# Performance work log

Measured on AMD Instinct MI355X. Metric: run time of the kernel, lower is better.

The kernel has to match this reference:

```python
import jax, jax.numpy as jnp
import numpy as np

D_MODEL = 1024
N_HEADS = 16
HEAD_DIM = D_MODEL // N_HEADS
BATCH = 4
SEQ = 2048


def setup_inputs() -> dict:
    key = jax.random.key(0)
    ks = jax.random.split(key, 5)
    # Xavier uniform bound for square d_model x d_model weights
    bound = np.sqrt(6.0 / (D_MODEL + D_MODEL))
    x = jax.random.normal(ks[0], (BATCH, SEQ, D_MODEL), dtype=jnp.float32)
    attention_mask = jnp.ones((BATCH, SEQ), dtype=jnp.int32)
    wq = jax.random.uniform(ks[1], (D_MODEL, D_MODEL), jnp.float32, -bound, bound)
    wk = jax.random.uniform(ks[2], (D_MODEL, D_MODEL), jnp.float32, -bound, bound)
    wv = jax.random.uniform(ks[3], (D_MODEL, D_MODEL), jnp.float32, -bound, bound)
    wo = jax.random.uniform(ks[4], (D_MODEL, D_MODEL), jnp.float32, -bound, bound)
    return {"x": x, "attention_mask": attention_mask,
            "wq": wq, "wk": wk, "wv": wv, "wo": wo}


def reference(x, attention_mask, wq, wk, wv, wo):
    # x: (B, S, D). Linear weights stored torch-style (out, in): y = x @ W^T
    B, S, D = x.shape
    H, Hd = N_HEADS, HEAD_DIM
    scale = np.sqrt(Hd).astype(np.float32)

    def split_heads(t):  # (B,S,D) -> (B,H,S,Hd)
        return t.reshape(B, S, H, Hd).transpose(0, 2, 1, 3)

    q = split_heads(jnp.einsum('bsd,ed->bse', x, wq))
    k = split_heads(jnp.einsum('bsd,ed->bse', x, wk))
    v = split_heads(jnp.einsum('bsd,ed->bse', x, wv))

    scores = jnp.einsum('bhqd,bhkd->bhqk', q, k) / scale  # (B,H,S,S)

    causal = jnp.tril(jnp.ones((S, S), dtype=bool))  # True = keep
    keep = causal[None, None, :, :] & (attention_mask[:, None, None, :] != 0)
    scores = jnp.where(keep, scores, -jnp.inf)

    attn = jax.nn.softmax(scores, axis=-1)  # dropout: eval mode (identity)
    out = jnp.einsum('bhqk,bhkd->bhqd', attn, v)  # (B,H,S,Hd)
    out = out.transpose(0, 2, 1, 3).reshape(B, S, D)
    return jnp.einsum('bsd,ed->bse', out, wo)
```

## Files before the change

### kernel.cpp

```cpp
#include <hip/hip_runtime.h>
#include <cstdint>
#include <cstddef>

#define D_MODEL 1024
#define N_HEADS 16
#define HEAD_DIM 64
#define BATCH 4
#define SEQ 2048
#define M_TOTAL (BATCH * SEQ)

typedef __attribute__((ext_vector_type(8))) short bf16x8;
typedef __attribute__((ext_vector_type(4))) float f32x4;
typedef __attribute__((ext_vector_type(16))) float f32x16;

#define Q_SCALE 0.18033688011112042f

__device__ __forceinline__ unsigned short f2bu(float f) {
    union { float f; unsigned u; } x; x.f = f;
    unsigned r = x.u + 0x7FFFu + ((x.u >> 16) & 1u);
    return (unsigned short)(r >> 16);
}

__device__ __forceinline__ void async16(void* lds, const void* g) {
    __builtin_amdgcn_global_load_lds(
        (const __attribute__((address_space(1))) void*)g,
        (__attribute__((address_space(3))) void*)lds, 16, 0, 0);
}

__global__ __launch_bounds__(256) void cast_all(const float* __restrict__ x,
                                                const float* __restrict__ wq,
                                                const float* __restrict__ wk,
                                                const float* __restrict__ wv,
                                                const float* __restrict__ wo,
                                                unsigned short* __restrict__ dst) {
    const size_t NE = (size_t)M_TOTAL * D_MODEL;
    const size_t WE = (size_t)D_MODEL * D_MODEL;
    size_t i4 = (size_t)blockIdx.x * 256 + threadIdx.x;
    size_t e = i4 * 4;
    const float* src; size_t off;
    if (e < NE) { src = x; off = e; }
    else {
        size_t t = e - NE;
        int r = (int)(t / WE); off = t - (size_t)r * WE;
        src = (r == 0) ? wq : (r == 1) ? wk : (r == 2) ? wv : wo;
    }
    float4 v = *(const float4*)(src + off);
    ushort4 o;
    o.x = f2bu(v.x); o.y = f2bu(v.y); o.z = f2bu(v.z); o.w = f2bu(v.w);
    ((ushort4*)dst)[i4] = o;
}

__global__ __launch_bounds__(256) void qkv_gemm(const unsigned short* __restrict__ X,
                                                const unsigned short* __restrict__ W0,
                                                const unsigned short* __restrict__ W1,
                                                const unsigned short* __restrict__ W2,
                                                unsigned short* __restrict__ Y0,
                                                unsigned short* __restrict__ Y1,
                                                unsigned short* __restrict__ Vt) {
    __shared__ short As[128 * 32];
    __shared__ short Bs[128 * 32];

    const int sel = blockIdx.x >> 3;
    const unsigned short* W = (sel == 0) ? W0 : (sel == 1) ? W1 : W2;
    const float scl = (sel == 0) ? Q_SCALE : 1.0f;

    const int tid = threadIdx.x;
    const int w = tid >> 6, lane = tid & 63, quad = lane >> 4, l15 = lane & 15;
    const int wm = w & 1, wn = w >> 1;
    const int rowBase = blockIdx.y * 128;
    const int colBase = (blockIdx.x & 7) * 128;

    f32x4 acc[4][4];
#pragma unroll
    for (int mi = 0; mi < 4; ++mi)
#pragma unroll
        for (int ni = 0; ni < 4; ++ni)
#pragma unroll
            for (int e = 0; e < 4; ++e) acc[mi][ni][e] = 0.f;

    for (int k0 = 0; k0 < 1024; k0 += 32) {
        __syncthreads();
#pragma unroll
        for (int l = 0; l < 2; ++l) {
            int c = tid + l * 256;
            int row = c >> 2, ccs = c & 3;
            int cc = ccs ^ ((row >> 1) & 3);
            async16((char*)As + c * 16, X + (size_t)(rowBase + row) * 1024 + k0 + cc * 8);
            async16((char*)Bs + c * 16, W + (size_t)(colBase + row) * 1024 + k0 + cc * 8);
        }
        __syncthreads();

        bf16x8 a[4], b[4];
#pragma unroll
        for (int mi = 0; mi < 4; ++mi) {
            int r = wm * 64 + mi * 16 + l15;
            int slot = quad ^ ((r >> 1) & 3);
            a[mi] = *(const bf16x8*)&As[r * 32 + slot * 8];
        }
#pragma unroll
        for (int ni = 0; ni < 4; ++ni) {
            int r = wn * 64 + ni * 16 + l15;
            int slot = quad ^ ((r >> 1) & 3);
            b[ni] = *(const bf16x8*)&Bs[r * 32 + slot * 8];
        }
#pragma unroll
        for (int mi = 0; mi < 4; ++mi)
#pragma unroll
            for (int ni = 0; ni < 4; ++ni)
                acc[mi][ni] = __builtin_amdgcn_mfma_f32_16x16x32_bf16(a[mi], b[ni], acc[mi][ni], 0, 0, 0);
    }

    if (sel != 2) {
        unsigned short* Y = (sel == 0) ? Y0 : Y1;
#pragma unroll
        for (int mi = 0; mi < 4; ++mi)
#pragma unroll
            for (int ni = 0; ni < 4; ++ni)
#pragma unroll
                for (int reg = 0; reg < 4; ++reg) {
                    int row = rowBase + wm * 64 + mi * 16 + quad * 4 + reg;
                    int col = colBase + wn * 64 + ni * 16 + l15;
                    Y[(size_t)row * 1024 + col] = f2bu(acc[mi][ni][reg] * scl);
                }
    } else {
#pragma unroll
        for (int mi = 0; mi < 4; ++mi) {
            int row0 = rowBase + wm * 64 + mi * 16 + quad * 4;
            int bb = row0 >> 11;
            int s0 = row0 & 2047;
#pragma unroll
            for (int ni = 0; ni < 4; ++ni) {
                int col = colBase + wn * 64 + ni * 16 + l15;
                int hh = col >> 6, dd = col & 63;
                ushort4 pk;
                pk.x = f2bu(acc[mi][ni][0]); pk.y = f2bu(acc[mi][ni][1]);
                pk.z = f2bu(acc[mi][ni][2]); pk.w = f2bu(acc[mi][ni][3]);
                *(ushort4*)(Vt + (((size_t)bb * 16 + hh) * 64 + dd) * SEQ + s0) = pk;
            }
        }
    }
}

__global__ __launch_bounds__(256) void out_gemm(const unsigned short* __restrict__ X,
                                                const unsigned short* __restrict__ W,
                                                float* __restrict__ Y) {
    __shared__ short As[128 * 32];
    __shared__ short Bs[128 * 32];

    const int tid = threadIdx.x;
    const int w = tid >> 6, lane = tid & 63, quad = lane >> 4, l15 = lane & 15;
    const int wm = w & 1, wn = w >> 1;
    const int rowBase = blockIdx.y * 128;
    const int colBase = blockIdx.x * 128;

    f32x4 acc[4][4];
#pragma unroll
    for (int mi = 0; mi < 4; ++mi)
#pragma unroll
        for (int ni = 0; ni < 4; ++ni)
#pragma unroll
            for (int e = 0; e < 4; ++e) acc[mi][ni][e] = 0.f;

    for (int k0 = 0; k0 < 1024; k0 += 32) {
        __syncthreads();
#pragma unroll
        for (int l = 0; l < 2; ++l) {
            int c = tid + l * 256;
            int row = c >> 2, ccs = c & 3;
            int cc = ccs ^ ((row >> 1) & 3);
            async16((char*)As + c * 16, X + (size_t)(rowBase + row) * 1024 + k0 + cc * 8);
            async16((char*)Bs + c * 16, W + (size_t)(colBase + row) * 1024 + k0 + cc * 8);
        }
        __syncthreads();

        bf16x8 a[4], b[4];
#pragma unroll
        for (int mi = 0; mi < 4; ++mi) {
            int r = wm * 64 + mi * 16 + l15;
            int slot = quad ^ ((r >> 1) & 3);
            a[mi] = *(const bf16x8*)&As[r * 32 + slot * 8];
        }
#pragma unroll
        for (int ni = 0; ni < 4; ++ni) {
            int r = wn * 64 + ni * 16 + l15;
            int slot = quad ^ ((r >> 1) & 3);
            b[ni] = *(const bf16x8*)&Bs[r * 32 + slot * 8];
        }
#pragma unroll
        for (int mi = 0; mi < 4; ++mi)
#pragma unroll
            for (int ni = 0; ni < 4; ++ni)
                acc[mi][ni] = __builtin_amdgcn_mfma_f32_16x16x32_bf16(a[mi], b[ni], acc[mi][ni], 0, 0, 0);
    }

#pragma unroll
    for (int mi = 0; mi < 4; ++mi)
#pragma unroll
        for (int ni = 0; ni < 4; ++ni)
#pragma unroll
            for (int reg = 0; reg < 4; ++reg) {
                int row = rowBase + wm * 64 + mi * 16 + quad * 4 + reg;
                int col = colBase + wn * 64 + ni * 16 + l15;
                Y[(size_t)row * 1024 + col] = acc[mi][ni][reg];
            }
}

__global__ __launch_bounds__(256) void flash32(const unsigned short* __restrict__ Q,
                                               const unsigned short* __restrict__ K,
                                               const unsigned short* __restrict__ Vt,
                                               const int* __restrict__ mask,
                                               unsigned short* __restrict__ CTX) {
    __shared__ short lds[9216];
    __shared__ float biasS[64];
    __shared__ int allokS;
    __shared__ int okW[4];

    short* Ks = lds;
    short* Vs = lds + 4096;

    const int pid = blockIdx.x;
    const int bh = blockIdx.y;
    const int b = bh >> 4;
    const int tid = threadIdx.x;
    const int w = tid >> 6, lane = tid & 63, l31 = lane & 31, lane5 = lane >> 5;

    const size_t qkBase = (size_t)b * SEQ * D_MODEL + (size_t)(bh & 15) * HEAD_DIM;
    const size_t vtBase = (size_t)bh * HEAD_DIM * SEQ;

    {
        int ok = 1;
        for (int i = tid; i < SEQ; i += 256) ok &= (mask[b * SEQ + i] != 0);
        unsigned long long bal = __ballot(ok != 0);
        if (lane == 0) okW[w] = (bal == ~0ull) ? 1 : 0;
    }
    __syncthreads();
    const int allSeq = okW[0] & okW[1] & okW[2] & okW[3];

    int stp[2], stcc[2], stj[2];
#pragma unroll
    for (int l = 0; l < 2; ++l) {
        int c = tid + l * 256;
        int p = c >> 3, sl = c & 7;
        stp[l] = p;
        stcc[l] = sl ^ (p & 7);
        stj[l] = (p & 0x33) | ((p & 4) << 1) | ((p & 8) >> 1);
    }

    for (int phase = 0; phase < 2; ++phase) {
        const int qt = phase ? pid : 15 - pid;
        const int q0 = qt * 128;
        const int iq = q0 + w * 32 + l31;

        bf16x8 qf[4];
#pragma unroll
        for (int ks = 0; ks < 4; ++ks)
            qf[ks] = *(const bf16x8*)(Q + qkBase + (size_t)iq * D_MODEL + ks * 16 + lane5 * 8);

        float mv = -INFINITY, lv = 0.f;
        f32x16 Ot[2];
#pragma unroll
        for (int dt = 0; dt < 2; ++dt)
#pragma unroll
            for (int e = 0; e < 16; ++e) Ot[dt][e] = 0.f;

        const int ktmax = 2 * qt + 1;

        uint4 kreg[2], vreg[2];
        int mreg = 1;
        {
            const int k0 = 0;
#pragma unroll
            for (int l = 0; l < 2; ++l) {
                kreg[l] = *(const uint4*)(K + qkBase + (size_t)(k0 + stj[l]) * D_MODEL + stcc[l] * 8);
                vreg[l] = *(const uint4*)(Vt + vtBase + (size_t)stp[l] * SEQ + k0 + stcc[l] * 8);
            }
            if (!allSeq && tid < 64) mreg = mask[b * SEQ + k0 + tid];
        }

        for (int kt = 0; kt <= ktmax; ++kt) {
            const int k0 = kt * 64;
            __syncthreads();
#pragma unroll
            for (int l = 0; l < 2; ++l) {
                int c = tid + l * 256;
                *(uint4*)((char*)Ks + c * 16) = kreg[l];
                *(uint4*)((char*)Vs + c * 16) = vreg[l];
            }
            if (!allSeq && tid < 64) {
                biasS[tid] = mreg ? 0.f : -INFINITY;
                unsigned long long bal = __ballot(mreg != 0);
                if (tid == 0) allokS = (bal == ~0ull) ? 1 : 0;
            }
            if (kt < ktmax) {
                const int kn = k0 + 64;
#pragma unroll
                for (int l = 0; l < 2; ++l) {
                    kreg[l] = *(const uint4*)(K + qkBase + (size_t)(kn + stj[l]) * D_MODEL + stcc[l] * 8);
                    vreg[l] = *(const uint4*)(Vt + vtBase + (size_t)stp[l] * SEQ + kn + stcc[l] * 8);
                }
                if (!allSeq && tid < 64) mreg = mask[b * SEQ + kn + tid];
            }
            __syncthreads();

            if (64 * kt > q0 + 32 * w + 31) continue;

            f32x16 St[2];
#pragma unroll
            for (int T = 0; T < 2; ++T)
#pragma unroll
                for (int e = 0; e < 16; ++e) St[T][e] = 0.f;
            __builtin_amdgcn_s_setprio(1);
#pragma unroll
            for (int T = 0; T < 2; ++T)
#pragma unroll
                for (int ks = 0; ks < 4; ++ks) {
                    int p = T * 32 + l31;
                    int slot = (ks * 2 + lane5) ^ (p & 7);
                    bf16x8 a = *(const bf16x8*)&Ks[p * 64 + slot * 8];
                    St[T] = __builtin_amdgcn_mfma_f32_32x32x16_bf16(a, qf[ks], St[T], 0, 0, 0);
                }
            __builtin_amdgcn_s_setprio(0);

            const bool partial = (k0 + 63 > q0 + 32 * w);
            if (partial) {
#pragma unroll
                for (int T = 0; T < 2; ++T)
#pragma unroll
                    for (int r = 0; r < 16; ++r) {
                        int j = k0 + 32 * T + 16 * (r >> 3) + 8 * lane5 + (r & 7);
                        if (j > iq) St[T][r] = -INFINITY;
                    }
            }
            if (!allSeq && !allokS) {
#pragma unroll
                for (int T = 0; T < 2; ++T)
#pragma unroll
                    for (int r = 0; r < 16; ++r)
                        St[T][r] += biasS[32 * T + 16 * (r >> 3) + 8 * lane5 + (r & 7)];
            }

            float rm = -INFINITY;
#pragma unroll
            for (int T = 0; T < 2; ++T)
#pragma unroll
                for (int r = 0; r < 16; ++r) rm = fmaxf(rm, St[T][r]);
            rm = fmaxf(rm, __shfl_xor(rm, 32));
            float mn = fmaxf(mv, rm);
            if (mn > mv + 8.f) {
                float al = exp2f(mv - mn);
                lv *= al;
#pragma unroll
                for (int dt = 0; dt < 2; ++dt)
#pragma unroll
                    for (int e = 0; e < 16; ++e) Ot[dt][e] *= al;
                mv = mn;
            }
            float rs = 0.f;
#pragma unroll
            for (int T = 0; T < 2; ++T)
#pragma unroll
                for (int r = 0; r < 16; ++r) {
                    float pv = exp2f(St[T][r] - mv);
                    St[T][r] = pv;
                    rs += pv;
                }
            rs += __shfl_xor(rs, 32);
            lv += rs;

            bf16x8 pf[4];
#pragma unroll
            for (int t = 0; t < 4; ++t) {
                const int T = t >> 1, hb = t & 1;
                unsigned u0, u1, u2, u3;
                asm("v_cvt_pk_bf16_f32 %0, %1, %2" : "=v"(u0)
                    : "v"(St[T][hb * 8 + 0]), "v"(St[T][hb * 8 + 1]));
                asm("v_cvt_pk_bf16_f32 %0, %1, %2" : "=v"(u1)
                    : "v"(St[T][hb * 8 + 2]), "v"(St[T][hb * 8 + 3]));
                asm("v_cvt_pk_bf16_f32 %0, %1, %2" : "=v"(u2)
                    : "v"(St[T][hb * 8 + 4]), "v"(St[T][hb * 8 + 5]));
                asm("v_cvt_pk_bf16_f32 %0, %1, %2" : "=v"(u3)
                    : "v"(St[T][hb * 8 + 6]), "v"(St[T][hb * 8 + 7]));
                union { unsigned u[4]; bf16x8 v; } pk;
                pk.u[0] = u0; pk.u[1] = u1; pk.u[2] = u2; pk.u[3] = u3;
                pf[t] = pk.v;
            }

            __builtin_amdgcn_s_setprio(1);
#pragma unroll
            for (int dt = 0; dt < 2; ++dt)
#pragma unroll
                for (int t = 0; t < 4; ++t) {
                    int p = dt * 32 + l31;
                    int slot = (t * 2 + lane5) ^ (p & 7);
                    bf16x8 a = *(const bf16x8*)&Vs[p * 64 + slot * 8];
                    Ot[dt] = __builtin_amdgcn_mfma_f32_32x32x16_bf16(a, pf[t], Ot[dt], 0, 0, 0);
                }
            __builtin_amdgcn_s_setprio(0);
        }

        __syncthreads();
        const float inv = 1.f / lv;
#pragma unroll
        for (int dt = 0; dt < 2; ++dt)
#pragma unroll
            for (int k = 0; k < 8; ++k) {
                int r0 = 2 * k;
                int d = (r0 & 3) + 4 * lane5 + 8 * (r0 >> 2) + 32 * dt;
                unsigned lo = f2bu(Ot[dt][r0] * inv);
                unsigned hi = f2bu(Ot[dt][r0 + 1] * inv);
                *(unsigned*)&lds[(w * 32 + l31) * 72 + d] = lo | (hi << 16);
            }
        __syncthreads();
#pragma unroll
        for (int k = 0; k < 4; ++k) {
            int id = tid + k * 256;
            int r = id >> 3, cc = id & 7;
            uint4 v = *(const uint4*)&lds[r * 72 + cc * 8];
            *(uint4*)(CTX + qkBase + (size_t)(q0 + r) * D_MODEL + cc * 8) = v;
        }
    }
}

extern "C" void kernel_launch(void* const* d_in, const int* in_sizes, int n_in,
                              void* d_out, int out_size, void* d_ws, size_t ws_size,
                              hipStream_t stream) {
    const float* x  = (const float*)d_in[0];
    const int* mask = (const int*)d_in[1];
    const float* wq = (const float*)d_in[2];
    const float* wk = (const float*)d_in[3];
    const float* wv = (const float*)d_in[4];
    const float* wo = (const float*)d_in[5];
    float* out = (float*)d_out;

    const size_t NE = (size_t)M_TOTAL * D_MODEL;
    const size_t WE = (size_t)D_MODEL * D_MODEL;
    unsigned short* ws  = (unsigned short*)d_ws;
    unsigned short* xb  = ws;
    unsigned short* wqb = xb + NE;
    unsigned short* wkb = wqb + WE;
    unsigned short* wvb = wkb + WE;
    unsigned short* wob = wvb + WE;
    unsigned short* Qb  = wob + WE;
    unsigned short* Kb  = Qb + NE;
    unsigned short* Vtb = Kb + NE;
    unsigned short* CTX = Vtb + NE;

    cast_all<<<(int)((NE + 4 * WE) / 4 / 256), 256, 0, stream>>>(x, wq, wk, wv, wo, ws);

    qkv_gemm<<<dim3(24, M_TOTAL / 128), 256, 0, stream>>>(xb, wqb, wkb, wvb, Qb, Kb, Vtb);

    flash32<<<dim3(8, BATCH * N_HEADS), 256, 0, stream>>>(Qb, Kb, Vtb, mask, CTX);

    out_gemm<<<dim3(D_MODEL / 128, M_TOTAL / 128), 256, 0, stream>>>(CTX, wob, out);
}
```

Baseline: 309.3 us.

## Double-buffer K/V tiles in flash kernel and launch one block per query tile

```diff
diff --git a/kernel.cpp b/kernel.cpp
--- a/kernel.cpp
+++ b/kernel.cpp
@@ -210,16 +210,13 @@
                                                const unsigned short* __restrict__ Vt,
                                                const int* __restrict__ mask,
                                                unsigned short* __restrict__ CTX) {
-    __shared__ short lds[9216];
-    __shared__ float biasS[64];
-    __shared__ int allokS;
+    __shared__ short lds[16384];
+    __shared__ float biasS[2][64];
+    __shared__ int allokS[2];
     __shared__ int okW[4];
 
-    short* Ks = lds;
-    short* Vs = lds + 4096;
-
-    const int pid = blockIdx.x;
-    const int bh = blockIdx.y;
+    const int bh = blockIdx.x;
+    const int qt = 15 - (int)blockIdx.y;
     const int b = bh >> 4;
     const int tid = threadIdx.x;
     const int w = tid >> 6, lane = tid & 63, l31 = lane & 31, lane5 = lane >> 5;
@@ -246,178 +243,177 @@
         stj[l] = (p & 0x33) | ((p & 4) << 1) | ((p & 8) >> 1);
     }
 
-    for (int phase = 0; phase < 2; ++phase) {
-        const int qt = phase ? pid : 15 - pid;
-        const int q0 = qt * 128;
-        const int iq = q0 + w * 32 + l31;
-
-        bf16x8 qf[4];
-#pragma unroll
-        for (int ks = 0; ks < 4; ++ks)
-            qf[ks] = *(const bf16x8*)(Q + qkBase + (size_t)iq * D_MODEL + ks * 16 + lane5 * 8);
-
-        float mv = -INFINITY, lv = 0.f;
-        f32x16 Ot[2];
+    const int q0 = qt * 128;
+    const int iq = q0 + w * 32 + l31;
+
+    bf16x8 qf[4];
+#pragma unroll
+    for (int ks = 0; ks < 4; ++ks)
+        qf[ks] = *(const bf16x8*)(Q + qkBase + (size_t)iq * D_MODEL + ks * 16 + lane5 * 8);
+
+    float mv = -INFINITY, lv = 0.f;
+    f32x16 Ot[2];
+#pragma unroll
+    for (int dt = 0; dt < 2; ++dt)
+#pragma unroll
+        for (int e = 0; e < 16; ++e) Ot[dt][e] = 0.f;
+
+    const int ktmax = 2 * qt + 1;
+
+    uint4 kreg[2], vreg[2];
+    int mreg = 1;
+#pragma unroll
+    for (int l = 0; l < 2; ++l) {
+        kreg[l] = *(const uint4*)(K + qkBase + (size_t)stj[l] * D_MODEL + stcc[l] * 8);
+        vreg[l] = *(const uint4*)(Vt + vtBase + (size_t)stp[l] * SEQ + stcc[l] * 8);
+    }
+    if (!allSeq && tid < 64) mreg = mask[b * SEQ + tid];
+
+    for (int kt = 0; kt <= ktmax; ++kt) {
+        const int k0 = kt * 64;
+        const int buf = kt & 1;
+#pragma unroll
+        for (int l = 0; l < 2; ++l) {
+            int c = tid + l * 256;
+            *(uint4*)((char*)lds + buf * 8192 + c * 16) = kreg[l];
+            *(uint4*)((char*)lds + 16384 + buf * 8192 + c * 16) = vreg[l];
+        }
+        if (!allSeq && tid < 64) {
+            biasS[buf][tid] = mreg ? 0.f : -INFINITY;
+            unsigned long long bal = __ballot(mreg != 0);
+            if (tid == 0) allokS[buf] = (bal == ~0ull) ? 1 : 0;
+        }
+        if (kt < ktmax) {
+            const int kn = k0 + 64;
+#pragma unroll
+            for (int l = 0; l < 2; ++l) {
+                kreg[l] = *(const uint4*)(K + qkBase + (size_t)(kn + stj[l]) * D_MODEL + stcc[l] * 8);
+                vreg[l] = *(const uint4*)(Vt + vtBase + (size_t)stp[l] * SEQ + kn + stcc[l] * 8);
+            }
+            if (!allSeq && tid < 64) mreg = mask[b * SEQ + kn + tid];
+        }
+        __syncthreads();
+
+        if (64 * kt > q0 + 32 * w + 31) continue;
+
+        const short* Ks = lds + buf * 4096;
+        const short* Vs = lds + 8192 + buf * 4096;
+
+        f32x16 St[2];
+#pragma unroll
+        for (int T = 0; T < 2; ++T)
+#pragma unroll
+            for (int e = 0; e < 16; ++e) St[T][e] = 0.f;
+        __builtin_amdgcn_s_setprio(1);
+#pragma unroll
+        for (int T = 0; T < 2; ++T)
+#pragma unroll
+            for (int ks = 0; ks < 4; ++ks) {
+                int p = T * 32 + l31;
+                int slot = (ks * 2 + lane5) ^ (p & 7);
+                bf16x8 a = *(const bf16x8*)&Ks[p * 64 + slot * 8];
+                St[T] = __builtin_amdgcn_mfma_f32_32x32x16_bf16(a, qf[ks], St[T], 0, 0, 0);
+            }
+        __builtin_amdgcn_s_setprio(0);
+
+        const bool partial = (k0 + 63 > q0 + 32 * w);
+        if (partial) {
+#pragma unroll
+            for (int T = 0; T < 2; ++T)
+#pragma unroll
+                for (int r = 0; r < 16; ++r) {
+                    int j = k0 + 32 * T + 16 * (r >> 3) + 8 * lane5 + (r & 7);
+                    if (j > iq) St[T][r] = -INFINITY;
+                }
+        }
+        if (!allSeq && !allokS[buf]) {
+#pragma unroll
+            for (int T = 0; T < 2; ++T)
+#pragma unroll
+                for (int r = 0; r < 16; ++r)
+                    St[T][r] += biasS[buf][32 * T + 16 * (r >> 3) + 8 * lane5 + (r & 7)];
+        }
+
+        float t0[8];
+#pragma unroll
+        for (int r = 0; r < 8; ++r)
+            t0[r] = fmaxf(fmaxf(St[0][r], St[0][r + 8]), fmaxf(St[1][r], St[1][r + 8]));
+        float t1a = fmaxf(fmaxf(t0[0], t0[1]), fmaxf(t0[2], t0[3]));
+        float t1b = fmaxf(fmaxf(t0[4], t0[5]), fmaxf(t0[6], t0[7]));
+        float rm = fmaxf(t1a, t1b);
+        rm = fmaxf(rm, __shfl_xor(rm, 32));
+        float mn = fmaxf(mv, rm);
+        if (mn > mv + 8.f) {
+            float al = exp2f(mv - mn);
+            lv *= al;
+#pragma unroll
+            for (int dt = 0; dt < 2; ++dt)
+#pragma unroll
+                for (int e = 0; e < 16; ++e) Ot[dt][e] *= al;
+            mv = mn;
+        }
+        float rs = 0.f;
+#pragma unroll
+        for (int T = 0; T < 2; ++T)
+#pragma unroll
+            for (int r = 0; r < 16; ++r) {
+                float pv = exp2f(St[T][r] - mv);
+                St[T][r] = pv;
+                rs += pv;
+            }
+        rs += __shfl_xor(rs, 32);
+        lv += rs;
+
+        bf16x8 pf[4];
+#pragma unroll
+        for (int t = 0; t < 4; ++t) {
+            const int T = t >> 1, hb = t & 1;
+            unsigned u0, u1, u2, u3;
+            asm("v_cvt_pk_bf16_f32 %0, %1, %2" : "=v"(u0)
+                : "v"(St[T][hb * 8 + 0]), "v"(St[T][hb * 8 + 1]));
+            asm("v_cvt_pk_bf16_f32 %0, %1, %2" : "=v"(u1)
+                : "v"(St[T][hb * 8 + 2]), "v"(St[T][hb * 8 + 3]));
+            asm("v_cvt_pk_bf16_f32 %0, %1, %2" : "=v"(u2)
+                : "v"(St[T][hb * 8 + 4]), "v"(St[T][hb * 8 + 5]));
+            asm("v_cvt_pk_bf16_f32 %0, %1, %2" : "=v"(u3)
+                : "v"(St[T][hb * 8 + 6]), "v"(St[T][hb * 8 + 7]));
+            union { unsigned u[4]; bf16x8 v; } pk;
+            pk.u[0] = u0; pk.u[1] = u1; pk.u[2] = u2; pk.u[3] = u3;
+            pf[t] = pk.v;
+        }
+
+        __builtin_amdgcn_s_setprio(1);
 #pragma unroll
         for (int dt = 0; dt < 2; ++dt)
 #pragma unroll
-            for (int e = 0; e < 16; ++e) Ot[dt][e] = 0.f;
-
-        const int ktmax = 2 * qt + 1;
-
-        uint4 kreg[2], vreg[2];
-        int mreg = 1;
-        {
-            const int k0 = 0;
-#pragma unroll
-            for (int l = 0; l < 2; ++l) {
-                kreg[l] = *(const uint4*)(K + qkBase + (size_t)(k0 + stj[l]) * D_MODEL + stcc[l] * 8);
-                vreg[l] = *(const uint4*)(Vt + vtBase + (size_t)stp[l] * SEQ + k0 + stcc[l] * 8);
-            }
-            if (!allSeq && tid < 64) mreg = mask[b * SEQ + k0 + tid];
-        }
-
-        for (int kt = 0; kt <= ktmax; ++kt) {
-            const int k0 = kt * 64;
-            __syncthreads();
-#pragma unroll
-            for (int l = 0; l < 2; ++l) {
-                int c = tid + l * 256;
-                *(uint4*)((char*)Ks + c * 16) = kreg[l];
-                *(uint4*)((char*)Vs + c * 16) = vreg[l];
-            }
-            if (!allSeq && tid < 64) {
-                biasS[tid] = mreg ? 0.f : -INFINITY;
-                unsigned long long bal = __ballot(mreg != 0);
-                if (tid == 0) allokS = (bal == ~0ull) ? 1 : 0;
-            }
-            if (kt < ktmax) {
-                const int kn = k0 + 64;
-#pragma unroll
-                for (int l = 0; l < 2; ++l) {
-                    kreg[l] = *(const uint4*)(K + qkBase + (size_t)(kn + stj[l]) * D_MODEL + stcc[l] * 8);
-                    vreg[l] = *(const uint4*)(Vt + vtBase + (size_t)stp[l] * SEQ + kn + stcc[l] * 8);
-                }
-                if (!allSeq && tid < 64) mreg = mask[b * SEQ + kn + tid];
-            }
-            __syncthreads();
-
-            if (64 * kt > q0 + 32 * w + 31) continue;
-
-            f32x16 St[2];
-#pragma unroll
-            for (int T = 0; T < 2; ++T)
-#pragma unroll
-                for (int e = 0; e < 16; ++e) St[T][e] = 0.f;
-            __builtin_amdgcn_s_setprio(1);
-#pragma unroll
-            for (int T = 0; T < 2; ++T)
-#pragma unroll
-                for (int ks = 0; ks < 4; ++ks) {
-                    int p = T * 32 + l31;
-                    int slot = (ks * 2 + lane5) ^ (p & 7);
-                    bf16x8 a = *(const bf16x8*)&Ks[p * 64 + slot * 8];
-                    St[T] = __builtin_amdgcn_mfma_f32_32x32x16_bf16(a, qf[ks], St[T], 0, 0, 0);
-                }
-            __builtin_amdgcn_s_setprio(0);
-
-            const bool partial = (k0 + 63 > q0 + 32 * w);
-            if (partial) {
-#pragma unroll
-                for (int T = 0; T < 2; ++T)
-#pragma unroll
-                    for (int r = 0; r < 16; ++r) {
-                        int j = k0 + 32 * T + 16 * (r >> 3) + 8 * lane5 + (r & 7);
-                        if (j > iq) St[T][r] = -INFINITY;
-                    }
-            }
-            if (!allSeq && !allokS) {
-#pragma unroll
-                for (int T = 0; T < 2; ++T)
-#pragma unroll
-                    for (int r = 0; r < 16; ++r)
-                        St[T][r] += biasS[32 * T + 16 * (r >> 3) + 8 * lane5 + (r & 7)];
-            }
-
-            float rm = -INFINITY;
-#pragma unroll
-            for (int T = 0; T < 2; ++T)
-#pragma unroll
-                for (int r = 0; r < 16; ++r) rm = fmaxf(rm, St[T][r]);
-            rm = fmaxf(rm, __shfl_xor(rm, 32));
-            float mn = fmaxf(mv, rm);
-            if (mn > mv + 8.f) {
-                float al = exp2f(mv - mn);
-                lv *= al;
-#pragma unroll
-                for (int dt = 0; dt < 2; ++dt)
-#pragma unroll
-                    for (int e = 0; e < 16; ++e) Ot[dt][e] *= al;
-                mv = mn;
-            }
-            float rs = 0.f;
-#pragma unroll
-            for (int T = 0; T < 2; ++T)
-#pragma unroll
-                for (int r = 0; r < 16; ++r) {
-                    float pv = exp2f(St[T][r] - mv);
-                    St[T][r] = pv;
-                    rs += pv;
-                }
-            rs += __shfl_xor(rs, 32);
-            lv += rs;
-
-            bf16x8 pf[4];
-#pragma unroll
             for (int t = 0; t < 4; ++t) {
-                const int T = t >> 1, hb = t & 1;
-                unsigned u0, u1, u2, u3;
-                asm("v_cvt_pk_bf16_f32 %0, %1, %2" : "=v"(u0)
-                    : "v"(St[T][hb * 8 + 0]), "v"(St[T][hb * 8 + 1]));
-                asm("v_cvt_pk_bf16_f32 %0, %1, %2" : "=v"(u1)
-                    : "v"(St[T][hb * 8 + 2]), "v"(St[T][hb * 8 + 3]));
-                asm("v_cvt_pk_bf16_f32 %0, %1, %2" : "=v"(u2)
-                    : "v"(St[T][hb * 8 + 4]), "v"(St[T][hb * 8 + 5]));
-                asm("v_cvt_pk_bf16_f32 %0, %1, %2" : "=v"(u3)
-                    : "v"(St[T][hb * 8 + 6]), "v"(St[T][hb * 8 + 7]));
-                union { unsigned u[4]; bf16x8 v; } pk;
-                pk.u[0] = u0; pk.u[1] = u1; pk.u[2] = u2; pk.u[3] = u3;
-                pf[t] = pk.v;
-            }
-
-            __builtin_amdgcn_s_setprio(1);
-#pragma unroll
-            for (int dt = 0; dt < 2; ++dt)
-#pragma unroll
-                for (int t = 0; t < 4; ++t) {
-                    int p = dt * 32 + l31;
-                    int slot = (t * 2 + lane5) ^ (p & 7);
-                    bf16x8 a = *(const bf16x8*)&Vs[p * 64 + slot * 8];
-                    Ot[dt] = __builtin_amdgcn_mfma_f32_32x32x16_bf16(a, pf[t], Ot[dt], 0, 0, 0);
-                }
-            __builtin_amdgcn_s_setprio(0);
-        }
-
-        __syncthreads();
-        const float inv = 1.f / lv;
-#pragma unroll
-        for (int dt = 0; dt < 2; ++dt)
-#pragma unroll
-            for (int k = 0; k < 8; ++k) {
-                int r0 = 2 * k;
-                int d = (r0 & 3) + 4 * lane5 + 8 * (r0 >> 2) + 32 * dt;
-                unsigned lo = f2bu(Ot[dt][r0] * inv);
-                unsigned hi = f2bu(Ot[dt][r0 + 1] * inv);
-                *(unsigned*)&lds[(w * 32 + l31) * 72 + d] = lo | (hi << 16);
-            }
-        __syncthreads();
-#pragma unroll
-        for (int k = 0; k < 4; ++k) {
-            int id = tid + k * 256;
-            int r = id >> 3, cc = id & 7;
-            uint4 v = *(const uint4*)&lds[r * 72 + cc * 8];
-            *(uint4*)(CTX + qkBase + (size_t)(q0 + r) * D_MODEL + cc * 8) = v;
-        }
+                int p = dt * 32 + l31;
+                int slot = (t * 2 + lane5) ^ (p & 7);
+                bf16x8 a = *(const bf16x8*)&Vs[p * 64 + slot * 8];
+                Ot[dt] = __builtin_amdgcn_mfma_f32_32x32x16_bf16(a, pf[t], Ot[dt], 0, 0, 0);
+            }
+        __builtin_amdgcn_s_setprio(0);
+    }
+
+    __syncthreads();
+    const float inv = 1.f / lv;
+#pragma unroll
+    for (int dt = 0; dt < 2; ++dt)
+#pragma unroll
+        for (int k = 0; k < 8; ++k) {
+            int r0 = 2 * k;
+            int d = (r0 & 3) + 4 * lane5 + 8 * (r0 >> 2) + 32 * dt;
+            unsigned lo = f2bu(Ot[dt][r0] * inv);
+            unsigned hi = f2bu(Ot[dt][r0 + 1] * inv);
+            *(unsigned*)&lds[(w * 32 + l31) * 72 + d] = lo | (hi << 16);
+        }
+    __syncthreads();
+#pragma unroll
+    for (int k = 0; k < 4; ++k) {
+        int id = tid + k * 256;
+        int r = id >> 3, cc = id & 7;
+        uint4 v = *(const uint4*)&lds[r * 72 + cc * 8];
+        *(uint4*)(CTX + qkBase + (size_t)(q0 + r) * D_MODEL + cc * 8) = v;
     }
 }
 
@@ -449,7 +445,7 @@
 
     qkv_gemm<<<dim3(24, M_TOTAL / 128), 256, 0, stream>>>(xb, wqb, wkb, wvb, Qb, Kb, Vtb);
 
-    flash32<<<dim3(8, BATCH * N_HEADS), 256, 0, stream>>>(Qb, Kb, Vtb, mask, CTX);
+    flash32<<<dim3(64, 16), 256, 0, stream>>>(Qb, Kb, Vtb, mask, CTX);
 
     out_gemm<<<dim3(D_MODEL / 128, M_TOTAL / 128), 256, 0, stream>>>(CTX, wob, out);
 }
```

After: 326.7 us. +5.6%, slower.
